# Optimization experiments

Hardware: AMD Instinct MI355X
Metric: run time of the kernel (lower is better)

## Reference

```python
import jax, jax.numpy as jnp
import numpy as np
from jax import lax

B, L, F = 32, 2048, 76   # batch, seq_len, feat_dim
H = 128                  # conv hidden channels
D = 128                  # prototype dim (last 1x1 conv)
P = 128                  # number of prototypes
CLASS_SIZE = 2


def setup_inputs() -> dict:
    key = jax.random.key(0)
    ks = jax.random.split(key, 8)
    w = lambda k, shape: jax.random.normal(k, shape, jnp.float32) * 0.05
    return {
        "x": jax.random.normal(ks[0], (B, L, F), jnp.float32),
        "W1": w(ks[1], (H, F, 5)), "b1": jnp.zeros((H,), jnp.float32),
        "W2": w(ks[2], (H, H, 5)), "b2": jnp.zeros((H,), jnp.float32),
        "W3": w(ks[3], (H, H, 5)), "b3": jnp.zeros((H,), jnp.float32),
        "Wo1": w(ks[4], (D, H)), "bo1": jnp.zeros((D,), jnp.float32),
        "Wo2": w(ks[5], (D, D)), "bo2": jnp.zeros((D,), jnp.float32),
        "prototypes": jax.random.uniform(ks[6], (P, D), jnp.float32),
        "protop_classes": jnp.concatenate([jnp.zeros(P // 2, jnp.int32), jnp.ones(P // 2, jnp.int32)]),
    }


def _conv1d_same(h, W, b):
    # h: (B, C, L), W: (O, C, K=5), symmetric padding 2 == torch padding=k//2
    y = lax.conv_general_dilated(h, W, window_strides=(1,), padding=[(2, 2)],
                                 dimension_numbers=("NCW", "OIW", "NCW"))
    return y + b[None, :, None]


def _maxpool2(h):
    return lax.reduce_window(h, -jnp.inf, lax.max, (1, 1, 2), (1, 1, 2), "VALID")


def reference(x, W1, b1, W2, b2, W3, b3, Wo1, bo1, Wo2, bo2, prototypes, protop_classes):
    h = jnp.transpose(x, (0, 2, 1))  # (B, F, L)
    for W, b in ((W1, b1), (W2, b2), (W3, b3)):
        h = _maxpool2(jax.nn.relu(_conv1d_same(h, W, b)))
    # 1x1 convs as channel matmuls
    h = jax.nn.relu(jnp.einsum("bcl,oc->bol", h, Wo1) + bo1[None, :, None])
    h = jax.nn.relu(jnp.einsum("bcl,oc->bol", h, Wo2) + bo2[None, :, None])
    f = jnp.transpose(h, (0, 2, 1))  # (B, Lp=256, D)
    # l2_conv via ||a-b||^2 = ||a||^2 - 2 a.b + ||b||^2 (same math, GEMM form)
    d2 = (jnp.sum(f * f, axis=-1, keepdims=True)
          - 2.0 * jnp.einsum("bld,pd->blp", f, prototypes)
          + jnp.sum(prototypes * prototypes, axis=-1))  # (B, Lp, P)
    dis = jnp.sqrt(jnp.maximum(d2, 1e-12))
    min_dis = jnp.min(dis, axis=1)  # (B, P): min over patches
    # dis2sim, 'log' activation
    sim = jnp.log((min_dis + 1.0) / (min_dis + 1e-4))
    # init_weights: last_layer.weight[i,j] = 1 if protop_classes[j]==i else -0.5
    lw = jnp.where(protop_classes[None, :] == jnp.arange(CLASS_SIZE)[:, None], 1.0, -0.5)
    out = jax.nn.sigmoid(sim @ lw.T)  # (B, CLASS_SIZE)
    return out, min_dis
```

## Files before the change

kernel.cpp:

```cpp
#include <hip/hip_runtime.h>
#include <cmath>


typedef __attribute__((ext_vector_type(8))) short short8;
typedef __attribute__((ext_vector_type(4))) float f32x4;

__device__ __forceinline__ unsigned short f2bf(float v) {
    union { float f; unsigned u; } x; x.f = v;
    unsigned r = x.u + 0x7fffu + ((x.u >> 16) & 1u);
    return (unsigned short)(r >> 16);
}
__device__ __forceinline__ float bf2f(unsigned short b) {
    union { unsigned u; float f; } x; x.u = ((unsigned)b) << 16;
    return x.f;
}

__device__ void pack_conv_w(int t, int total, const float* __restrict__ W, int C,
                            unsigned short* __restrict__ dst)
{
    if (t >= total) return;
    int lane = t & 63, rest = t >> 6;
    int mf = rest & 7; rest >>= 3;
    int kk = rest % 5, cc = rest / 5;
    int m = mf * 16 + (lane & 15);
    int cb = cc * 32 + (lane >> 4) * 8;
    unsigned short v[8];
#pragma unroll
    for (int j = 0; j < 8; ++j) {
        int c = cb + j;
        v[j] = (c < C) ? f2bf(W[((size_t)m * C + c) * 5 + kk]) : (unsigned short)0;
    }
    *(uint4*)&dst[(size_t)t * 8] = *(uint4*)v;
}

__device__ void pack_mat(int t, const float* __restrict__ M, unsigned short* __restrict__ dst)
{
    if (t >= 2048) return;
    int lane = t & 63, mf = (t >> 6) & 7, cc = t >> 9;
    int m = mf * 16 + (lane & 15);
    int c0 = cc * 32 + (lane >> 4) * 8;
    unsigned short v[8];
#pragma unroll
    for (int j = 0; j < 8; ++j) v[j] = f2bf(M[(size_t)m * 128 + c0 + j]);
    *(uint4*)&dst[(size_t)t * 8] = *(uint4*)v;
}

__global__ __launch_bounds__(256)
void prep_weights_kernel(const float* __restrict__ W1, const float* __restrict__ W2,
                         const float* __restrict__ W3, const float* __restrict__ Wo1,
                         const float* __restrict__ Wo2, const float* __restrict__ protos,
                         unsigned short* A1, unsigned short* A2, unsigned short* A3,
                         unsigned short* AW1, unsigned short* AW2, unsigned short* AP,
                         float* pn, unsigned* pm_bits)
{
    int t = blockIdx.x * 256 + threadIdx.x;
    switch (blockIdx.y) {
    case 0: pack_conv_w(t, 7680,  W1, 76,  A1); break;
    case 1: pack_conv_w(t, 10240, W2, 128, A2); break;
    case 2: pack_conv_w(t, 10240, W3, 128, A3); break;
    case 3: pack_mat(t, Wo1, AW1); break;
    case 4: pack_mat(t, Wo2, AW2); break;
    case 5: pack_mat(t, protos, AP); break;
    case 6:
        if (t < 128) {
            float s = 0.f;
            for (int d = 0; d < 128; ++d) {
                float v = bf2f(f2bf(protos[(size_t)t * 128 + d]));
                s = fmaf(v, v, s);
            }
            pn[t] = s;
        }
        break;
    case 7:
        if (t < 4096) pm_bits[t] = 0x7F800000u;
        break;
    }
}

template <int MF, int NJ, int NCC, int STRIDE, int ROWMAX>
__device__ __forceinline__ void conv_k(const unsigned short* __restrict__ Af,
                                       const unsigned short* __restrict__ sIn,
                                       int nbase, int mf0, int lane,
                                       f32x4 (&acc)[MF][NJ])
{
    const int lc = lane & 15;
    const int lk = (lane >> 4) * 8;
#pragma unroll
    for (int i = 0; i < MF; ++i)
#pragma unroll
        for (int j = 0; j < NJ; ++j) acc[i][j] = (f32x4){0.f, 0.f, 0.f, 0.f};

    for (int cc = 0; cc < NCC; ++cc) {
#pragma unroll
        for (int kk = 0; kk < 5; ++kk) {
            const int step = cc * 5 + kk;
            short8 a[MF];
#pragma unroll
            for (int i = 0; i < MF; ++i)
                a[i] = *(const short8*)&Af[(((size_t)step * 8 + mf0 + i) * 64 + lane) * 8];
            short8 bb[NJ];
#pragma unroll
            for (int j = 0; j < NJ; ++j) {
                int row = nbase + j * 16 + lc + kk;
                if (ROWMAX >= 0) row = min(row, ROWMAX);
                bb[j] = *(const short8*)&sIn[row * STRIDE + cc * 32 + lk];
            }
#pragma unroll
            for (int j = 0; j < NJ; ++j)
#pragma unroll
                for (int i = 0; i < MF; ++i)
                    acc[i][j] = __builtin_amdgcn_mfma_f32_16x16x32_bf16(a[i], bb[j], acc[i][j], 0, 0, 0);
        }
    }
}

__device__ __forceinline__ void gemm_head(const unsigned short* __restrict__ Af,
                                          const unsigned short* __restrict__ s_in,
                                          int mf0h, int lane, f32x4 (&acc)[2])
{
    const int lc = lane & 15;
    const int lk = (lane >> 4) * 8;
    acc[0] = (f32x4){0.f, 0.f, 0.f, 0.f};
    acc[1] = (f32x4){0.f, 0.f, 0.f, 0.f};
#pragma unroll
    for (int cc = 0; cc < 4; ++cc) {
        short8 a[2];
#pragma unroll
        for (int i = 0; i < 2; ++i)
            a[i] = *(const short8*)&Af[(((size_t)cc * 8 + mf0h + i) * 64 + lane) * 8];
        short8 bb = *(const short8*)&s_in[lc * 136 + cc * 32 + lk];
#pragma unroll
        for (int i = 0; i < 2; ++i)
            acc[i] = __builtin_amdgcn_mfma_f32_16x16x32_bf16(a[i], bb, acc[i], 0, 0, 0);
    }
}

__global__ __launch_bounds__(256) __attribute__((amdgpu_waves_per_eu(4, 4)))
void mega_kernel(const float* __restrict__ x,
                 const unsigned short* __restrict__ A1, const float* __restrict__ b1,
                 const unsigned short* __restrict__ A2, const float* __restrict__ b2,
                 const unsigned short* __restrict__ A3, const float* __restrict__ b3,
                 const unsigned short* __restrict__ AW1, const float* __restrict__ bo1,
                 const unsigned short* __restrict__ AW2, const float* __restrict__ bo2,
                 const unsigned short* __restrict__ AP,  const float* __restrict__ pn,
                 unsigned* __restrict__ pm_bits)
{
    __shared__ __align__(16) unsigned short s_x[100 * 104];
    __shared__ __align__(16) unsigned short s_h1[44 * 136];
    __shared__ float s_cb[768];
    __shared__ float s_part[64];
    __shared__ float s_fn[16];
    unsigned short* s_h2 = s_x;
    unsigned short* s_f  = s_x + 2720;

    const int tid  = threadIdx.x;
    const int u    = blockIdx.x;
    const int b    = blockIdx.y;
    const int lane = tid & 63;
    const int wid  = tid >> 6;
    const int mf0  = wid * 2;
    const int lc   = lane & 15;
    const int lq   = (lane >> 4) * 4;

    for (int i = tid; i < 768; i += 256) {
        const float* src = (i < 128) ? b1 : (i < 256) ? b2 : (i < 384) ? b3
                         : (i < 512) ? bo1 : (i < 640) ? bo2 : pn;
        s_cb[i] = src[i & 127];
    }

    const int xbase = 64 * u - 14;
    for (int idx = tid; idx < 100 * 24; idx += 256) {
        int pos = idx / 24, c0 = (idx % 24) * 4;
        int l = xbase + pos;
        unsigned short v[4] = {0, 0, 0, 0};
        if (c0 < 76 && l >= 0 && l < 2048) {
            float4 xv = *(const float4*)&x[((size_t)b * 2048 + l) * 76 + c0];
            v[0] = f2bf(xv.x); v[1] = f2bf(xv.y); v[2] = f2bf(xv.z); v[3] = f2bf(xv.w);
        }
        *(uint2*)&s_x[pos * 104 + c0] = *(uint2*)v;
    }
    __syncthreads();

    {
        f32x4 acc[2][6];
        conv_k<2, 6, 3, 104, -1>(A1, s_x, 0, mf0, lane, acc);

#pragma unroll
        for (int i = 0; i < 2; ++i) {
            const int ch0 = (mf0 + i) * 16 + lq;
#pragma unroll
            for (int j = 0; j < 6; ++j) {
                const int nl = j * 16 + lc;
                unsigned short pk[4];
#pragma unroll
                for (int r = 0; r < 4; ++r) {
                    float v = fmaxf(acc[i][j][r] + s_cb[ch0 + r], 0.f);
                    float o = __shfl_xor(v, 1);
                    pk[r] = f2bf(fmaxf(v, o));
                }
                if ((lc & 1) == 0) {
                    int rr = nl >> 1;
                    int jg = 32 * u - 6 + rr;
                    if (rr < 44) {
                        uint2 val = (jg >= 0 && jg < 1024) ? *(uint2*)pk : make_uint2(0u, 0u);
                        *(uint2*)&s_h1[rr * 136 + ch0] = val;
                    }
                }
            }
        }
    }
    __syncthreads();

    {
        if (tid < 136) ((uint4*)(s_f + 8 * 136))[tid] = make_uint4(0u, 0u, 0u, 0u);

        f32x4 acc[2][3];
        conv_k<2, 3, 4, 136, 43>(A2, s_h1, 0, mf0, lane, acc);

#pragma unroll
        for (int i = 0; i < 2; ++i) {
            const int ch0 = (mf0 + i) * 16 + lq;
#pragma unroll
            for (int j = 0; j < 3; ++j) {
                const int nl = j * 16 + lc;
                unsigned short pk[4];
#pragma unroll
                for (int r = 0; r < 4; ++r) {
                    float v = fmaxf(acc[i][j][r] + s_cb[128 + ch0 + r], 0.f);
                    float o = __shfl_xor(v, 1);
                    pk[r] = f2bf(fmaxf(v, o));
                }
                if ((lc & 1) == 0) {
                    int rr = nl >> 1;
                    int jg = 16 * u - 2 + rr;
                    if (rr < 20) {
                        uint2 val = (jg >= 0 && jg < 512) ? *(uint2*)pk : make_uint2(0u, 0u);
                        *(uint2*)&s_h2[rr * 136 + ch0] = val;
                    }
                }
            }
        }
    }
    __syncthreads();

    {
        f32x4 acc[2][1];
        conv_k<2, 1, 4, 136, -1>(A3, s_h2, 0, mf0, lane, acc);

#pragma unroll
        for (int i = 0; i < 2; ++i) {
            const int ch0 = (mf0 + i) * 16 + lq;
            unsigned short pk[4];
#pragma unroll
            for (int r = 0; r < 4; ++r) {
                float v = fmaxf(acc[i][0][r] + s_cb[256 + ch0 + r], 0.f);
                float o = __shfl_xor(v, 1);
                pk[r] = f2bf(fmaxf(v, o));
            }
            if ((lc & 1) == 0)
                *(uint2*)&s_f[(lc >> 1) * 136 + ch0] = *(uint2*)pk;
        }
    }
    __syncthreads();

    f32x4 hacc[2];

    gemm_head(AW1, s_f, mf0, lane, hacc);
    __syncthreads();
#pragma unroll
    for (int i = 0; i < 2; ++i) {
        const int ch0 = (mf0 + i) * 16 + lq;
        unsigned short pk[4];
#pragma unroll
        for (int r = 0; r < 4; ++r)
            pk[r] = f2bf(fmaxf(hacc[i][r] + s_cb[384 + ch0 + r], 0.f));
        *(uint2*)&s_f[lc * 136 + ch0] = *(uint2*)pk;
    }
    __syncthreads();

    gemm_head(AW2, s_f, mf0, lane, hacc);
    __syncthreads();
#pragma unroll
    for (int i = 0; i < 2; ++i) {
        const int ch0 = (mf0 + i) * 16 + lq;
        unsigned short pk[4];
#pragma unroll
        for (int r = 0; r < 4; ++r)
            pk[r] = f2bf(fmaxf(hacc[i][r] + s_cb[512 + ch0 + r], 0.f));
        *(uint2*)&s_f[lc * 136 + ch0] = *(uint2*)pk;
    }
    __syncthreads();

    if (tid < 64) {
        int n = tid >> 2, part = tid & 3;
        float s = 0.f;
        for (int c = part * 32; c < part * 32 + 32; ++c) {
            float v = bf2f(s_f[n * 136 + c]);
            s = fmaf(v, v, s);
        }
        s_part[part * 16 + n] = s;
    }
    __syncthreads();
    if (tid < 16)
        s_fn[tid] = s_part[tid] + s_part[16 + tid] + s_part[32 + tid] + s_part[48 + tid];
    __syncthreads();

    gemm_head(AP, s_f, mf0, lane, hacc);

#pragma unroll
    for (int i = 0; i < 2; ++i) {
#pragma unroll
        for (int r = 0; r < 4; ++r) {
            const int p = (mf0 + i) * 16 + lq + r;
            float d2 = s_fn[lc] + s_cb[640 + p] - 2.f * hacc[i][r];
            float m = sqrtf(fmaxf(d2, 1e-12f));
#pragma unroll
            for (int s = 1; s < 8; s <<= 1)
                m = fminf(m, __shfl_xor(m, s));
            if (lc == 0)
                atomicMin(&pm_bits[(size_t)b * 128 + p], __float_as_uint(m));
        }
    }
}

__global__ __launch_bounds__(128)
void finalize_kernel(const float* __restrict__ pm,
                     const int* __restrict__ classes,
                     float* __restrict__ out)
{
    __shared__ float r0[128], r1[128];
    const int b = blockIdx.x, p = threadIdx.x;
    float m = pm[(size_t)b * 128 + p];
    out[64 + b * 128 + p] = m;

    float sim = logf((m + 1.0f) / (m + 1e-4f));
    int cls = classes[p];
    r0[p] = (cls == 0) ? sim : -0.5f * sim;
    r1[p] = (cls == 1) ? sim : -0.5f * sim;
    __syncthreads();
    for (int s = 64; s > 0; s >>= 1) {
        if (p < s) { r0[p] += r0[p + s]; r1[p] += r1[p + s]; }
        __syncthreads();
    }
    if (p == 0) {
        out[b * 2 + 0] = 1.f / (1.f + expf(-r0[0]));
        out[b * 2 + 1] = 1.f / (1.f + expf(-r1[0]));
    }
}

extern "C" void kernel_launch(void* const* d_in, const int* in_sizes, int n_in,
                              void* d_out, int out_size, void* d_ws, size_t ws_size,
                              hipStream_t stream)
{
    (void)in_sizes; (void)n_in; (void)out_size; (void)ws_size;
    const float* x    = (const float*)d_in[0];
    const float* W1   = (const float*)d_in[1];
    const float* b1   = (const float*)d_in[2];
    const float* W2   = (const float*)d_in[3];
    const float* b2   = (const float*)d_in[4];
    const float* W3   = (const float*)d_in[5];
    const float* b3   = (const float*)d_in[6];
    const float* Wo1  = (const float*)d_in[7];
    const float* bo1  = (const float*)d_in[8];
    const float* Wo2  = (const float*)d_in[9];
    const float* bo2  = (const float*)d_in[10];
    const float* prot = (const float*)d_in[11];
    const int*   cls  = (const int*)d_in[12];
    float* out = (float*)d_out;

    char* ws = (char*)d_ws;
    unsigned short* A1  = (unsigned short*)(ws);
    unsigned short* A2  = (unsigned short*)(ws + 122880);
    unsigned short* A3  = (unsigned short*)(ws + 286720);
    unsigned short* AW1 = (unsigned short*)(ws + 450560);
    unsigned short* AW2 = (unsigned short*)(ws + 483328);
    unsigned short* AP  = (unsigned short*)(ws + 516096);
    float*          pn  = (float*)(ws + 548864);
    unsigned*       pm  = (unsigned*)(ws + 549376);

    prep_weights_kernel<<<dim3(40, 8), 256, 0, stream>>>(W1, W2, W3, Wo1, Wo2, prot,
                                                         A1, A2, A3, AW1, AW2, AP, pn, pm);
    mega_kernel<<<dim3(32, 32), 256, 0, stream>>>(x, A1, b1, A2, b2, A3, b3,
                                                  AW1, bo1, AW2, bo2, AP, pn, pm);
    finalize_kernel<<<32, 128, 0, stream>>>((const float*)pm, cls, out);
}
```

Measured before the change: 127.8 us.

## Use 512-thread blocks with one M-fragment per wave in mega kernel

Doubles the fused kernel's block size from 4 to 8 waves, so each wave owns a single 16-channel output fragment instead of two in every conv and head GEMM stage. This shortens each wave's serial MFMA chain and adds more waves to hide latency. In exchange each wave reloads the shared-memory B operand for only one A fragment, so LDS traffic per MFMA doubles, and the launch bounds change from a fixed waves-per-EU hint to 512 threads.

```diff
diff --git a/kernel.cpp b/kernel.cpp
--- a/kernel.cpp
+++ b/kernel.cpp
@@ -114,28 +114,22 @@
     }
 }
 
-__device__ __forceinline__ void gemm_head(const unsigned short* __restrict__ Af,
-                                          const unsigned short* __restrict__ s_in,
-                                          int mf0h, int lane, f32x4 (&acc)[2])
+__device__ __forceinline__ void gemm_head1(const unsigned short* __restrict__ Af,
+                                           const unsigned short* __restrict__ s_in,
+                                           int mf, int lane, f32x4 &acc)
 {
     const int lc = lane & 15;
     const int lk = (lane >> 4) * 8;
-    acc[0] = (f32x4){0.f, 0.f, 0.f, 0.f};
-    acc[1] = (f32x4){0.f, 0.f, 0.f, 0.f};
+    acc = (f32x4){0.f, 0.f, 0.f, 0.f};
 #pragma unroll
     for (int cc = 0; cc < 4; ++cc) {
-        short8 a[2];
-#pragma unroll
-        for (int i = 0; i < 2; ++i)
-            a[i] = *(const short8*)&Af[(((size_t)cc * 8 + mf0h + i) * 64 + lane) * 8];
+        short8 a = *(const short8*)&Af[(((size_t)cc * 8 + mf) * 64 + lane) * 8];
         short8 bb = *(const short8*)&s_in[lc * 136 + cc * 32 + lk];
-#pragma unroll
-        for (int i = 0; i < 2; ++i)
-            acc[i] = __builtin_amdgcn_mfma_f32_16x16x32_bf16(a[i], bb, acc[i], 0, 0, 0);
-    }
-}
-
-__global__ __launch_bounds__(256) __attribute__((amdgpu_waves_per_eu(4, 4)))
+        acc = __builtin_amdgcn_mfma_f32_16x16x32_bf16(a, bb, acc, 0, 0, 0);
+    }
+}
+
+__global__ __launch_bounds__(512, 8)
 void mega_kernel(const float* __restrict__ x,
                  const unsigned short* __restrict__ A1, const float* __restrict__ b1,
                  const unsigned short* __restrict__ A2, const float* __restrict__ b2,
@@ -158,18 +152,18 @@
     const int b    = blockIdx.y;
     const int lane = tid & 63;
     const int wid  = tid >> 6;
-    const int mf0  = wid * 2;
+    const int mf   = wid;
     const int lc   = lane & 15;
     const int lq   = (lane >> 4) * 4;
 
-    for (int i = tid; i < 768; i += 256) {
+    for (int i = tid; i < 768; i += 512) {
         const float* src = (i < 128) ? b1 : (i < 256) ? b2 : (i < 384) ? b3
                          : (i < 512) ? bo1 : (i < 640) ? bo2 : pn;
         s_cb[i] = src[i & 127];
     }
 
     const int xbase = 64 * u - 14;
-    for (int idx = tid; idx < 100 * 24; idx += 256) {
+    for (int idx = tid; idx < 100 * 24; idx += 512) {
         int pos = idx / 24, c0 = (idx % 24) * 4;
         int l = xbase + pos;
         unsigned short v[4] = {0, 0, 0, 0};
@@ -182,111 +176,100 @@
     __syncthreads();
 
     {
-        f32x4 acc[2][6];
-        conv_k<2, 6, 3, 104, -1>(A1, s_x, 0, mf0, lane, acc);
-
-#pragma unroll
-        for (int i = 0; i < 2; ++i) {
-            const int ch0 = (mf0 + i) * 16 + lq;
-#pragma unroll
-            for (int j = 0; j < 6; ++j) {
-                const int nl = j * 16 + lc;
-                unsigned short pk[4];
-#pragma unroll
-                for (int r = 0; r < 4; ++r) {
-                    float v = fmaxf(acc[i][j][r] + s_cb[ch0 + r], 0.f);
-                    float o = __shfl_xor(v, 1);
-                    pk[r] = f2bf(fmaxf(v, o));
-                }
-                if ((lc & 1) == 0) {
-                    int rr = nl >> 1;
-                    int jg = 32 * u - 6 + rr;
-                    if (rr < 44) {
-                        uint2 val = (jg >= 0 && jg < 1024) ? *(uint2*)pk : make_uint2(0u, 0u);
-                        *(uint2*)&s_h1[rr * 136 + ch0] = val;
-                    }
-                }
-            }
-        }
-    }
-    __syncthreads();
-
-    {
-        if (tid < 136) ((uint4*)(s_f + 8 * 136))[tid] = make_uint4(0u, 0u, 0u, 0u);
-
-        f32x4 acc[2][3];
-        conv_k<2, 3, 4, 136, 43>(A2, s_h1, 0, mf0, lane, acc);
-
-#pragma unroll
-        for (int i = 0; i < 2; ++i) {
-            const int ch0 = (mf0 + i) * 16 + lq;
-#pragma unroll
-            for (int j = 0; j < 3; ++j) {
-                const int nl = j * 16 + lc;
-                unsigned short pk[4];
-#pragma unroll
-                for (int r = 0; r < 4; ++r) {
-                    float v = fmaxf(acc[i][j][r] + s_cb[128 + ch0 + r], 0.f);
-                    float o = __shfl_xor(v, 1);
-                    pk[r] = f2bf(fmaxf(v, o));
-                }
-                if ((lc & 1) == 0) {
-                    int rr = nl >> 1;
-                    int jg = 16 * u - 2 + rr;
-                    if (rr < 20) {
-                        uint2 val = (jg >= 0 && jg < 512) ? *(uint2*)pk : make_uint2(0u, 0u);
-                        *(uint2*)&s_h2[rr * 136 + ch0] = val;
-                    }
-                }
-            }
-        }
-    }
-    __syncthreads();
-
-    {
-        f32x4 acc[2][1];
-        conv_k<2, 1, 4, 136, -1>(A3, s_h2, 0, mf0, lane, acc);
-
-#pragma unroll
-        for (int i = 0; i < 2; ++i) {
-            const int ch0 = (mf0 + i) * 16 + lq;
+        f32x4 acc[1][6];
+        conv_k<1, 6, 3, 104, -1>(A1, s_x, 0, mf, lane, acc);
+
+        const int ch0 = mf * 16 + lq;
+#pragma unroll
+        for (int j = 0; j < 6; ++j) {
+            const int nl = j * 16 + lc;
             unsigned short pk[4];
 #pragma unroll
             for (int r = 0; r < 4; ++r) {
-                float v = fmaxf(acc[i][0][r] + s_cb[256 + ch0 + r], 0.f);
+                float v = fmaxf(acc[0][j][r] + s_cb[ch0 + r], 0.f);
                 float o = __shfl_xor(v, 1);
                 pk[r] = f2bf(fmaxf(v, o));
             }
-            if ((lc & 1) == 0)
-                *(uint2*)&s_f[(lc >> 1) * 136 + ch0] = *(uint2*)pk;
-        }
-    }
-    __syncthreads();
-
-    f32x4 hacc[2];
-
-    gemm_head(AW1, s_f, mf0, lane, hacc);
-    __syncthreads();
-#pragma unroll
-    for (int i = 0; i < 2; ++i) {
-        const int ch0 = (mf0 + i) * 16 + lq;
+            if ((lc & 1) == 0) {
+                int rr = nl >> 1;
+                int jg = 32 * u - 6 + rr;
+                if (rr < 44) {
+                    uint2 val = (jg >= 0 && jg < 1024) ? *(uint2*)pk : make_uint2(0u, 0u);
+                    *(uint2*)&s_h1[rr * 136 + ch0] = val;
+                }
+            }
+        }
+    }
+    __syncthreads();
+
+    {
+        if (tid < 136) ((uint4*)(s_f + 8 * 136))[tid] = make_uint4(0u, 0u, 0u, 0u);
+
+        f32x4 acc[1][3];
+        conv_k<1, 3, 4, 136, 43>(A2, s_h1, 0, mf, lane, acc);
+
+        const int ch0 = mf * 16 + lq;
+#pragma unroll
+        for (int j = 0; j < 3; ++j) {
+            const int nl = j * 16 + lc;
+            unsigned short pk[4];
+#pragma unroll
+            for (int r = 0; r < 4; ++r) {
+                float v = fmaxf(acc[0][j][r] + s_cb[128 + ch0 + r], 0.f);
+                float o = __shfl_xor(v, 1);
+                pk[r] = f2bf(fmaxf(v, o));
+            }
+            if ((lc & 1) == 0) {
+                int rr = nl >> 1;
+                int jg = 16 * u - 2 + rr;
+                if (rr < 20) {
+                    uint2 val = (jg >= 0 && jg < 512) ? *(uint2*)pk : make_uint2(0u, 0u);
+                    *(uint2*)&s_h2[rr * 136 + ch0] = val;
+                }
+            }
+        }
+    }
+    __syncthreads();
+
+    {
+        f32x4 acc[1][1];
+        conv_k<1, 1, 4, 136, -1>(A3, s_h2, 0, mf, lane, acc);
+
+        const int ch0 = mf * 16 + lq;
         unsigned short pk[4];
 #pragma unroll
+        for (int r = 0; r < 4; ++r) {
+            float v = fmaxf(acc[0][0][r] + s_cb[256 + ch0 + r], 0.f);
+            float o = __shfl_xor(v, 1);
+            pk[r] = f2bf(fmaxf(v, o));
+        }
+        if ((lc & 1) == 0)
+            *(uint2*)&s_f[(lc >> 1) * 136 + ch0] = *(uint2*)pk;
+    }
+    __syncthreads();
+
+    f32x4 hacc;
+
+    gemm_head1(AW1, s_f, mf, lane, hacc);
+    __syncthreads();
+    {
+        const int ch0 = mf * 16 + lq;
+        unsigned short pk[4];
+#pragma unroll
         for (int r = 0; r < 4; ++r)
-            pk[r] = f2bf(fmaxf(hacc[i][r] + s_cb[384 + ch0 + r], 0.f));
+            pk[r] = f2bf(fmaxf(hacc[r] + s_cb[384 + ch0 + r], 0.f));
         *(uint2*)&s_f[lc * 136 + ch0] = *(uint2*)pk;
     }
     __syncthreads();
 
-    gemm_head(AW2, s_f, mf0, lane, hacc);
-    __syncthreads();
-#pragma unroll
-    for (int i = 0; i < 2; ++i) {
-        const int ch0 = (mf0 + i) * 16 + lq;
+    gemm_head1(AW2, s_f, mf, lane, hacc);
+    __syncthreads();
+    {
+        const int ch0 = mf * 16 + lq;
         unsigned short pk[4];
 #pragma unroll
         for (int r = 0; r < 4; ++r)
-            pk[r] = f2bf(fmaxf(hacc[i][r] + s_cb[512 + ch0 + r], 0.f));
+            pk[r] = f2bf(fmaxf(hacc[r] + s_cb[512 + ch0 + r], 0.f));
         *(uint2*)&s_f[lc * 136 + ch0] = *(uint2*)pk;
     }
     __syncthreads();
@@ -305,21 +288,18 @@
         s_fn[tid] = s_part[tid] + s_part[16 + tid] + s_part[32 + tid] + s_part[48 + tid];
     __syncthreads();
 
-    gemm_head(AP, s_f, mf0, lane, hacc);
-
-#pragma unroll
-    for (int i = 0; i < 2; ++i) {
-#pragma unroll
-        for (int r = 0; r < 4; ++r) {
-            const int p = (mf0 + i) * 16 + lq + r;
-            float d2 = s_fn[lc] + s_cb[640 + p] - 2.f * hacc[i][r];
-            float m = sqrtf(fmaxf(d2, 1e-12f));
-#pragma unroll
-            for (int s = 1; s < 8; s <<= 1)
-                m = fminf(m, __shfl_xor(m, s));
-            if (lc == 0)
-                atomicMin(&pm_bits[(size_t)b * 128 + p], __float_as_uint(m));
-        }
+    gemm_head1(AP, s_f, mf, lane, hacc);
+
+#pragma unroll
+    for (int r = 0; r < 4; ++r) {
+        const int p = mf * 16 + lq + r;
+        float d2 = s_fn[lc] + s_cb[640 + p] - 2.f * hacc[r];
+        float m = sqrtf(fmaxf(d2, 1e-12f));
+#pragma unroll
+        for (int s = 1; s < 8; s <<= 1)
+            m = fminf(m, __shfl_xor(m, s));
+        if (lc == 0)
+            atomicMin(&pm_bits[(size_t)b * 128 + p], __float_as_uint(m));
     }
 }
 
@@ -380,7 +360,7 @@
 
     prep_weights_kernel<<<dim3(40, 8), 256, 0, stream>>>(W1, W2, W3, Wo1, Wo2, prot,
                                                          A1, A2, A3, AW1, AW2, AP, pn, pm);
-    mega_kernel<<<dim3(32, 32), 256, 0, stream>>>(x, A1, b1, A2, b2, A3, b3,
+    mega_kernel<<<dim3(32, 32), 512, 0, stream>>>(x, A1, b1, A2, b2, A3, b3,
                                                   AW1, bo1, AW2, bo2, AP, pn, pm);
     finalize_kernel<<<32, 128, 0, stream>>>((const float*)pm, cls, out);
 }
```

After: 129.0 us. Within noise of the previous version (+0.9%).

## Halve per-block sequence tile and double grid; read biases directly from global

Applied to the files above, without the earlier changes.

Each block now covers 32 input positions instead of 64, so it yields 4 final patches instead of 8. The grid doubles to 64x32 blocks and shared-memory buffers shrink accordingly. The LDS bias/norm staging buffer is removed in favour of vector loads straight from global memory, and the waves_per_eu attribute is dropped. The aim is more parallelism and occupancy, at the cost of relatively more redundant halo computation and head GEMM rows that carry no useful output per block.

```diff
diff --git a/kernel.cpp b/kernel.cpp
--- a/kernel.cpp
+++ b/kernel.cpp
@@ -135,7 +135,7 @@
     }
 }
 
-__global__ __launch_bounds__(256) __attribute__((amdgpu_waves_per_eu(4, 4)))
+__global__ __launch_bounds__(256)
 void mega_kernel(const float* __restrict__ x,
                  const unsigned short* __restrict__ A1, const float* __restrict__ b1,
                  const unsigned short* __restrict__ A2, const float* __restrict__ b2,
@@ -145,13 +145,12 @@
                  const unsigned short* __restrict__ AP,  const float* __restrict__ pn,
                  unsigned* __restrict__ pm_bits)
 {
-    __shared__ __align__(16) unsigned short s_x[100 * 104];
-    __shared__ __align__(16) unsigned short s_h1[44 * 136];
-    __shared__ float s_cb[768];
-    __shared__ float s_part[64];
-    __shared__ float s_fn[16];
+    __shared__ __align__(16) unsigned short s_x[60 * 104];
+    __shared__ __align__(16) unsigned short s_h1[28 * 136];
     unsigned short* s_h2 = s_x;
-    unsigned short* s_f  = s_x + 2720;
+    unsigned short* s_f  = s_x + 1632;
+    float* s_part = (float*)(s_x + 3840);
+    float* s_fn   = (float*)(s_x + 3968);
 
     const int tid  = threadIdx.x;
     const int u    = blockIdx.x;
@@ -162,14 +161,8 @@
     const int lc   = lane & 15;
     const int lq   = (lane >> 4) * 4;
 
-    for (int i = tid; i < 768; i += 256) {
-        const float* src = (i < 128) ? b1 : (i < 256) ? b2 : (i < 384) ? b3
-                         : (i < 512) ? bo1 : (i < 640) ? bo2 : pn;
-        s_cb[i] = src[i & 127];
-    }
-
-    const int xbase = 64 * u - 14;
-    for (int idx = tid; idx < 100 * 24; idx += 256) {
+    const int xbase = 32 * u - 14;
+    for (int idx = tid; idx < 60 * 24; idx += 256) {
         int pos = idx / 24, c0 = (idx % 24) * 4;
         int l = xbase + pos;
         unsigned short v[4] = {0, 0, 0, 0};
@@ -182,26 +175,27 @@
     __syncthreads();
 
     {
-        f32x4 acc[2][6];
-        conv_k<2, 6, 3, 104, -1>(A1, s_x, 0, mf0, lane, acc);
+        f32x4 acc[2][4];
+        conv_k<2, 4, 3, 104, 59>(A1, s_x, 0, mf0, lane, acc);
 
 #pragma unroll
         for (int i = 0; i < 2; ++i) {
             const int ch0 = (mf0 + i) * 16 + lq;
-#pragma unroll
-            for (int j = 0; j < 6; ++j) {
+            const f32x4 bv = *(const f32x4*)&b1[ch0];
+#pragma unroll
+            for (int j = 0; j < 4; ++j) {
                 const int nl = j * 16 + lc;
                 unsigned short pk[4];
 #pragma unroll
                 for (int r = 0; r < 4; ++r) {
-                    float v = fmaxf(acc[i][j][r] + s_cb[ch0 + r], 0.f);
+                    float v = fmaxf(acc[i][j][r] + bv[r], 0.f);
                     float o = __shfl_xor(v, 1);
                     pk[r] = f2bf(fmaxf(v, o));
                 }
                 if ((lc & 1) == 0) {
                     int rr = nl >> 1;
-                    int jg = 32 * u - 6 + rr;
-                    if (rr < 44) {
+                    int jg = 16 * u - 6 + rr;
+                    if (rr < 28) {
                         uint2 val = (jg >= 0 && jg < 1024) ? *(uint2*)pk : make_uint2(0u, 0u);
                         *(uint2*)&s_h1[rr * 136 + ch0] = val;
                     }
@@ -212,28 +206,29 @@
     __syncthreads();
 
     {
-        if (tid < 136) ((uint4*)(s_f + 8 * 136))[tid] = make_uint4(0u, 0u, 0u, 0u);
-
-        f32x4 acc[2][3];
-        conv_k<2, 3, 4, 136, 43>(A2, s_h1, 0, mf0, lane, acc);
+        if (tid < 204) ((uint4*)(s_f + 4 * 136))[tid] = make_uint4(0u, 0u, 0u, 0u);
+
+        f32x4 acc[2][2];
+        conv_k<2, 2, 4, 136, 27>(A2, s_h1, 0, mf0, lane, acc);
 
 #pragma unroll
         for (int i = 0; i < 2; ++i) {
             const int ch0 = (mf0 + i) * 16 + lq;
-#pragma unroll
-            for (int j = 0; j < 3; ++j) {
+            const f32x4 bv = *(const f32x4*)&b2[ch0];
+#pragma unroll
+            for (int j = 0; j < 2; ++j) {
                 const int nl = j * 16 + lc;
                 unsigned short pk[4];
 #pragma unroll
                 for (int r = 0; r < 4; ++r) {
-                    float v = fmaxf(acc[i][j][r] + s_cb[128 + ch0 + r], 0.f);
+                    float v = fmaxf(acc[i][j][r] + bv[r], 0.f);
                     float o = __shfl_xor(v, 1);
                     pk[r] = f2bf(fmaxf(v, o));
                 }
                 if ((lc & 1) == 0) {
                     int rr = nl >> 1;
-                    int jg = 16 * u - 2 + rr;
-                    if (rr < 20) {
+                    int jg = 8 * u - 2 + rr;
+                    if (rr < 12) {
                         uint2 val = (jg >= 0 && jg < 512) ? *(uint2*)pk : make_uint2(0u, 0u);
                         *(uint2*)&s_h2[rr * 136 + ch0] = val;
                     }
@@ -245,19 +240,20 @@
 
     {
         f32x4 acc[2][1];
-        conv_k<2, 1, 4, 136, -1>(A3, s_h2, 0, mf0, lane, acc);
+        conv_k<2, 1, 4, 136, 11>(A3, s_h2, 0, mf0, lane, acc);
 
 #pragma unroll
         for (int i = 0; i < 2; ++i) {
             const int ch0 = (mf0 + i) * 16 + lq;
+            const f32x4 bv = *(const f32x4*)&b3[ch0];
             unsigned short pk[4];
 #pragma unroll
             for (int r = 0; r < 4; ++r) {
-                float v = fmaxf(acc[i][0][r] + s_cb[256 + ch0 + r], 0.f);
+                float v = fmaxf(acc[i][0][r] + bv[r], 0.f);
                 float o = __shfl_xor(v, 1);
                 pk[r] = f2bf(fmaxf(v, o));
             }
-            if ((lc & 1) == 0)
+            if ((lc & 1) == 0 && lc < 8)
                 *(uint2*)&s_f[(lc >> 1) * 136 + ch0] = *(uint2*)pk;
         }
     }
@@ -270,10 +266,11 @@
 #pragma unroll
     for (int i = 0; i < 2; ++i) {
         const int ch0 = (mf0 + i) * 16 + lq;
+        const f32x4 bv = *(const f32x4*)&bo1[ch0];
         unsigned short pk[4];
 #pragma unroll
         for (int r = 0; r < 4; ++r)
-            pk[r] = f2bf(fmaxf(hacc[i][r] + s_cb[384 + ch0 + r], 0.f));
+            pk[r] = f2bf(fmaxf(hacc[i][r] + bv[r], 0.f));
         *(uint2*)&s_f[lc * 136 + ch0] = *(uint2*)pk;
     }
     __syncthreads();
@@ -283,10 +280,11 @@
 #pragma unroll
     for (int i = 0; i < 2; ++i) {
         const int ch0 = (mf0 + i) * 16 + lq;
+        const f32x4 bv = *(const f32x4*)&bo2[ch0];
         unsigned short pk[4];
 #pragma unroll
         for (int r = 0; r < 4; ++r)
-            pk[r] = f2bf(fmaxf(hacc[i][r] + s_cb[512 + ch0 + r], 0.f));
+            pk[r] = f2bf(fmaxf(hacc[i][r] + bv[r], 0.f));
         *(uint2*)&s_f[lc * 136 + ch0] = *(uint2*)pk;
     }
     __syncthreads();
@@ -309,13 +307,14 @@
 
 #pragma unroll
     for (int i = 0; i < 2; ++i) {
+        const f32x4 pnv = *(const f32x4*)&pn[(mf0 + i) * 16 + lq];
 #pragma unroll
         for (int r = 0; r < 4; ++r) {
             const int p = (mf0 + i) * 16 + lq + r;
-            float d2 = s_fn[lc] + s_cb[640 + p] - 2.f * hacc[i][r];
+            float d2 = s_fn[lc] + pnv[r] - 2.f * hacc[i][r];
             float m = sqrtf(fmaxf(d2, 1e-12f));
 #pragma unroll
-            for (int s = 1; s < 8; s <<= 1)
+            for (int s = 1; s < 4; s <<= 1)
                 m = fminf(m, __shfl_xor(m, s));
             if (lc == 0)
                 atomicMin(&pm_bits[(size_t)b * 128 + p], __float_as_uint(m));
@@ -380,7 +379,7 @@
 
     prep_weights_kernel<<<dim3(40, 8), 256, 0, stream>>>(W1, W2, W3, Wo1, Wo2, prot,
                                                          A1, A2, A3, AW1, AW2, AP, pn, pm);
-    mega_kernel<<<dim3(32, 32), 256, 0, stream>>>(x, A1, b1, A2, b2, A3, b3,
+    mega_kernel<<<dim3(64, 32), 256, 0, stream>>>(x, A1, b1, A2, b2, A3, b3,
                                                   AW1, bo1, AW2, bo2, AP, pn, pm);
     finalize_kernel<<<32, 128, 0, stream>>>((const float*)pm, cls, out);
 }
```

Measured after the change: 155.7 us. 21.8% more time.
